# Performance work log

Measured on AMD Instinct MI355X. Metric: run time of the kernel, lower is better.

## Reference

```python
import jax, jax.numpy as jnp
import numpy as np

N = 100000
FEAT = 256
HID = 128
OUT = 64
E = 1600000


def setup_inputs() -> dict:
    key = jax.random.key(0)
    ks = jax.random.split(key, 8)
    x = jax.random.normal(ks[0], (N, FEAT), dtype=jnp.float32)
    edge_index = jax.random.randint(ks[1], (2, E), 0, N, dtype=jnp.int64)
    # Glorot-like weights, zero bias (PyG GCNConv default init style)
    def glorot(k, fin, fout):
        s = (6.0 / (fin + fout)) ** 0.5
        return jax.random.uniform(k, (fin, fout), jnp.float32, -s, s)
    return {
        "x": x,
        "edge_index": edge_index,
        "W1": glorot(ks[2], FEAT, HID), "b1": jnp.zeros((HID,), jnp.float32),
        "W2": glorot(ks[3], HID, HID), "b2": jnp.zeros((HID,), jnp.float32),
        "W3": glorot(ks[4], HID, OUT), "b3": jnp.zeros((OUT,), jnp.float32),
    }


def _gcn_prep(edge_index, n_nodes):
    # Add self-loops and compute symmetric normalization deg^-1/2 (PyG gcn_norm).
    loops = jnp.arange(n_nodes, dtype=edge_index.dtype)
    src = jnp.concatenate([edge_index[0], loops])
    dst = jnp.concatenate([edge_index[1], loops])
    ones = jnp.ones(src.shape[0], dtype=jnp.float32)
    deg = jax.ops.segment_sum(ones, dst, num_segments=n_nodes)
    dinv = jnp.where(deg > 0, jax.lax.rsqrt(jnp.maximum(deg, 1.0)), 0.0)
    norm = dinv[src] * dinv[dst]  # [E+N]
    return src, dst, norm


def _gcn_layer(x, src, dst, norm, W, b, n_nodes):
    h = x @ W                              # [N, F_out]
    msg = h[src] * norm[:, None]           # gather + edge scale
    out = jax.ops.segment_sum(msg, dst, num_segments=n_nodes)  # scatter-add
    return out + b


def reference(x, edge_index, W1, b1, W2, b2, W3, b3):
    n = x.shape[0]
    src, dst, norm = _gcn_prep(edge_index, n)
    h = jax.nn.relu(_gcn_layer(x, src, dst, norm, W1, b1, n))
    h = jax.nn.relu(_gcn_layer(h, src, dst, norm, W2, b2, n))
    return _gcn_layer(h, src, dst, norm, W3, b3, n)
```

## Files before the change

### kernel.cpp

```cpp
#include <hip/hip_runtime.h>
#include <hip/hip_bf16.h>


#define NNODES 100000
#define NB 391
#define PB 2048
#define BCAP 12288

typedef _Float16 half8  __attribute__((ext_vector_type(8)));
typedef _Float16 half4v __attribute__((ext_vector_type(4)));
typedef _Float16 half2v __attribute__((ext_vector_type(2)));
typedef float    floatx4 __attribute__((ext_vector_type(4)));

static __device__ __forceinline__ floatx4 h2f4(half4v v) {
    return (floatx4){(float)v.x, (float)v.y, (float)v.z, (float)v.w};
}

__global__ __launch_bounds__(256) void blockhist_k(const int* __restrict__ dst,
                                                   int* __restrict__ H, int e) {
    __shared__ int h[NB];
    for (int q = threadIdx.x; q < NB; q += 256) h[q] = 0;
    __syncthreads();
    int base = blockIdx.x * PB;
    int lim = e - base; if (lim > PB) lim = PB;
    for (int i = threadIdx.x; i < lim; i += 256)
        atomicAdd(&h[dst[base + i] >> 8], 1);
    __syncthreads();
    for (int q = threadIdx.x; q < NB; q += 256)
        H[(size_t)blockIdx.x * NB + q] = h[q];
}

__global__ __launch_bounds__(256) void bucketscan_k(const int* __restrict__ H,
                                                    int* __restrict__ O,
                                                    int* __restrict__ T, int npb) {
    __shared__ int lds[256];
    int b = blockIdx.x, t = threadIdx.x;
    int running = 0;
    for (int c0 = 0; c0 < npb; c0 += 256) {
        int idx = c0 + t;
        int v = (idx < npb) ? H[(size_t)idx * NB + b] : 0;
        lds[t] = v;
        __syncthreads();
        #pragma unroll
        for (int off = 1; off < 256; off <<= 1) {
            int u = (t >= off) ? lds[t - off] : 0;
            __syncthreads();
            lds[t] += u;
            __syncthreads();
        }
        int excl = lds[t] - v + running;
        if (idx < npb) O[(size_t)idx * NB + b] = excl;
        running += lds[255];
        __syncthreads();
    }
    if (t == 0) T[b] = running;
}

__global__ __launch_bounds__(512) void scanT_k(const int* __restrict__ T,
                                               int* __restrict__ bbase, int e) {
    __shared__ int lds[512];
    int t = threadIdx.x;
    int v = (t < NB) ? T[t] : 0;
    lds[t] = v;
    __syncthreads();
    #pragma unroll
    for (int off = 1; off < 512; off <<= 1) {
        int u = (t >= off) ? lds[t - off] : 0;
        __syncthreads();
        lds[t] += u;
        __syncthreads();
    }
    if (t < NB) bbase[t] = lds[t] - v;
    if (t == 0) bbase[NB] = e;
}

__global__ __launch_bounds__(256) void scatter_k(const int* __restrict__ src,
                                                 const int* __restrict__ dst,
                                                 const int* __restrict__ O,
                                                 const int* __restrict__ bbase,
                                                 unsigned* __restrict__ binned, int e) {
    __shared__ int cur[NB];
    for (int q = threadIdx.x; q < NB; q += 256)
        cur[q] = bbase[q] + O[(size_t)blockIdx.x * NB + q];
    __syncthreads();
    int base = blockIdx.x * PB;
    int lim = e - base; if (lim > PB) lim = PB;
    for (int i = threadIdx.x; i < lim; i += 256) {
        int d = dst[base + i];
        int s = src[base + i];
        int p = atomicAdd(&cur[d >> 8], 1);
        binned[p] = ((unsigned)(d & 255) << 17) | (unsigned)s;
    }
}

__global__ __launch_bounds__(256) void bucket_fill_k(
    const unsigned* __restrict__ binned, const int* __restrict__ bbase,
    int* __restrict__ rowptr, int* __restrict__ eidx,
    float* __restrict__ dinv, int n, int e) {
    __shared__ int cnt[256];
    __shared__ int cur[256];
    __shared__ int lds[256];
    __shared__ int sbuf[BCAP];
    int b = blockIdx.x, t = threadIdx.x;
    int beg = bbase[b], end = bbase[b + 1];
    int m = end - beg;
    cnt[t] = 0;
    __syncthreads();
    for (int q = t; q < m; q += 256) {
        unsigned r = binned[beg + q];
        atomicAdd(&cnt[r >> 17], 1);
    }
    __syncthreads();
    int v = cnt[t];
    lds[t] = v;
    __syncthreads();
    #pragma unroll
    for (int off = 1; off < 256; off <<= 1) {
        int u = (t >= off) ? lds[t - off] : 0;
        __syncthreads();
        lds[t] += u;
        __syncthreads();
    }
    int excl = lds[t] - v;
    int node = b * 256 + t;
    if (node < n) {
        rowptr[node] = beg + excl;
        dinv[node] = rsqrtf(1.0f + (float)v);
    }
    if (b == NB - 1 && t == 0) rowptr[n] = e;
    cur[t] = excl;
    __syncthreads();
    for (int q = t; q < m; q += 256) {
        unsigned r = binned[beg + q];
        int p = atomicAdd(&cur[r >> 17], 1);
        if (p < BCAP) sbuf[p] = (int)(r & 0x1FFFFu);
    }
    __syncthreads();
    for (int q = t; q < m; q += 256) eidx[beg + q] = sbuf[q];
}

template<typename TA, int FIN, int FOUT>
__global__ __launch_bounds__(256) void gemm_mfma_k(
    const TA* __restrict__ X, const float* __restrict__ W,
    const float* __restrict__ dinv, _Float16* __restrict__ G, int n)
{
    constexpr int KC = (FIN > 128) ? 128 : FIN;
    constexpr int KP = KC + 8;
    constexpr int NT = FOUT / 16;
    __shared__ _Float16 wT[FOUT * KP];

    const int tid  = threadIdx.x;
    const int wave = tid >> 6;
    const int lane = tid & 63;
    const int mrow = lane & 15;
    const int kq   = (lane >> 4) * 8;

    const int m0 = blockIdx.x * 128 + wave * 32;
    int r0 = m0 + mrow;      if (r0 > n - 1) r0 = n - 1;
    int r1 = m0 + 16 + mrow; if (r1 > n - 1) r1 = n - 1;

    floatx4 acc[2][NT];
    #pragma unroll
    for (int i = 0; i < 2; ++i)
        #pragma unroll
        for (int j = 0; j < NT; ++j) acc[i][j] = (floatx4){0.f, 0.f, 0.f, 0.f};

    for (int kc = 0; kc < FIN; kc += KC) {
        if (kc) __syncthreads();
        for (int q = tid; q < KC * FOUT; q += 256) {
            int k = q / FOUT, nn = q % FOUT;
            wT[nn * KP + k] = (_Float16)W[(size_t)(kc + k) * FOUT + nn];
        }
        __syncthreads();

        #pragma unroll
        for (int kk = 0; kk < KC; kk += 32) {
            half8 a0, a1;
            if constexpr (sizeof(TA) == 2) {
                const _Float16* xp = (const _Float16*)X;
                a0 = *(const half8*)(xp + (size_t)r0 * FIN + kc + kk + kq);
                a1 = *(const half8*)(xp + (size_t)r1 * FIN + kc + kk + kq);
            } else {
                const float* xp0 = (const float*)X + (size_t)r0 * FIN + kc + kk + kq;
                const float* xp1 = (const float*)X + (size_t)r1 * FIN + kc + kk + kq;
                float4 u0 = *(const float4*)xp0, u1 = *(const float4*)(xp0 + 4);
                float4 v0 = *(const float4*)xp1, v1 = *(const float4*)(xp1 + 4);
                a0 = (half8){(_Float16)u0.x, (_Float16)u0.y, (_Float16)u0.z, (_Float16)u0.w,
                             (_Float16)u1.x, (_Float16)u1.y, (_Float16)u1.z, (_Float16)u1.w};
                a1 = (half8){(_Float16)v0.x, (_Float16)v0.y, (_Float16)v0.z, (_Float16)v0.w,
                             (_Float16)v1.x, (_Float16)v1.y, (_Float16)v1.z, (_Float16)v1.w};
            }
            #pragma unroll
            for (int ct = 0; ct < NT; ++ct) {
                half8 b = *(const half8*)&wT[(ct * 16 + mrow) * KP + kk + kq];
                acc[0][ct] = __builtin_amdgcn_mfma_f32_16x16x32_f16(a0, b, acc[0][ct], 0, 0, 0);
                acc[1][ct] = __builtin_amdgcn_mfma_f32_16x16x32_f16(a1, b, acc[1][ct], 0, 0, 0);
            }
        }
    }

    #pragma unroll
    for (int rt = 0; rt < 2; ++rt) {
        #pragma unroll
        for (int reg = 0; reg < 4; ++reg) {
            int r = m0 + rt * 16 + (lane >> 4) * 4 + reg;
            if (r < n) {
                float s = dinv[r];
                #pragma unroll
                for (int ct = 0; ct < NT; ++ct) {
                    G[(size_t)r * FOUT + ct * 16 + mrow] = (_Float16)(acc[rt][ct][reg] * s);
                }
            }
        }
    }
}

template<bool RELU, typename OutT>
__global__ __launch_bounds__(256) void gather128_k(
    const _Float16* __restrict__ g, const int* __restrict__ rowptr,
    const int* __restrict__ eidx, const float* __restrict__ dinv,
    const float* __restrict__ bias, OutT* __restrict__ out, int n)
{
    int wave = threadIdx.x >> 6;
    int lane = threadIdx.x & 63;
    int half = lane >> 5;
    int hl   = lane & 31;
    int node = blockIdx.x * 4 + wave;
    if (node >= n) return;

    int beg = rowptr[node];
    int end = rowptr[node + 1];

    const half4v* g4 = (const half4v*)g;
    floatx4 aA = {0.f,0.f,0.f,0.f}, aB = aA, aC = aA, aD = aA;
    if (half == 0) aA = h2f4(g4[(size_t)node * 32 + hl]);

    for (int j0 = beg; j0 < end; j0 += 64) {
        int m = end - j0; if (m > 64) m = 64;
        int id = (lane < m) ? eidx[j0 + lane] : 0;
        int t = 0;
        for (; t + 7 < m; t += 8) {
            int i0 = __shfl(id, t + half);
            int i1 = __shfl(id, t + 2 + half);
            int i2 = __shfl(id, t + 4 + half);
            int i3 = __shfl(id, t + 6 + half);
            half4v v0 = g4[(size_t)i0 * 32 + hl];
            half4v v1 = g4[(size_t)i1 * 32 + hl];
            half4v v2 = g4[(size_t)i2 * 32 + hl];
            half4v v3 = g4[(size_t)i3 * 32 + hl];
            aA += h2f4(v0); aB += h2f4(v1); aC += h2f4(v2); aD += h2f4(v3);
        }
        for (; t + 1 < m; t += 2) {
            int i0 = __shfl(id, t + half);
            aA += h2f4(g4[(size_t)i0 * 32 + hl]);
        }
        if (t < m) {
            int i0 = __shfl(id, t);
            if (half == 0) aA += h2f4(g4[(size_t)i0 * 32 + hl]);
        }
    }
    aA += aB; aC += aD; aA += aC;
    aA.x += __shfl_down(aA.x, 32);
    aA.y += __shfl_down(aA.y, 32);
    aA.z += __shfl_down(aA.z, 32);
    aA.w += __shfl_down(aA.w, 32);

    if (half == 0) {
        float sc = dinv[node];
        float4 bb = *(const float4*)(bias + 4 * hl);
        float o0 = fmaf(aA.x, sc, bb.x);
        float o1 = fmaf(aA.y, sc, bb.y);
        float o2 = fmaf(aA.z, sc, bb.z);
        float o3 = fmaf(aA.w, sc, bb.w);
        if (RELU) {
            o0 = fmaxf(o0, 0.f); o1 = fmaxf(o1, 0.f);
            o2 = fmaxf(o2, 0.f); o3 = fmaxf(o3, 0.f);
        }
        if constexpr (sizeof(OutT) == 2) {
            ((half4v*)out)[(size_t)node * 32 + hl] =
                (half4v){(_Float16)o0, (_Float16)o1, (_Float16)o2, (_Float16)o3};
        } else {
            *(float4*)((float*)out + (size_t)node * 128 + 4 * hl) =
                make_float4(o0, o1, o2, o3);
        }
    }
}

template<bool RELU>
__global__ __launch_bounds__(256) void gather64_k(
    const _Float16* __restrict__ g, const int* __restrict__ rowptr,
    const int* __restrict__ eidx, const float* __restrict__ dinv,
    const float* __restrict__ bias, float* __restrict__ out, int n)
{
    int wave = threadIdx.x >> 6;
    int lane = threadIdx.x & 63;
    int half = lane >> 5;
    int hl   = lane & 31;
    int node = blockIdx.x * 4 + wave;
    if (node >= n) return;

    int beg = rowptr[node];
    int end = rowptr[node + 1];

    const half2v* g2 = (const half2v*)g;
    float ax=0.f, ay=0.f, bx=0.f, by=0.f, cx=0.f, cy=0.f, dx=0.f, dy=0.f;
    if (half == 0) {
        half2v v = g2[(size_t)node * 32 + hl];
        ax = (float)v.x; ay = (float)v.y;
    }

    for (int j0 = beg; j0 < end; j0 += 64) {
        int m = end - j0; if (m > 64) m = 64;
        int id = (lane < m) ? eidx[j0 + lane] : 0;
        int t = 0;
        for (; t + 7 < m; t += 8) {
            int i0 = __shfl(id, t + half);
            int i1 = __shfl(id, t + 2 + half);
            int i2 = __shfl(id, t + 4 + half);
            int i3 = __shfl(id, t + 6 + half);
            half2v v0 = g2[(size_t)i0 * 32 + hl];
            half2v v1 = g2[(size_t)i1 * 32 + hl];
            half2v v2 = g2[(size_t)i2 * 32 + hl];
            half2v v3 = g2[(size_t)i3 * 32 + hl];
            ax += (float)v0.x; ay += (float)v0.y;
            bx += (float)v1.x; by += (float)v1.y;
            cx += (float)v2.x; cy += (float)v2.y;
            dx += (float)v3.x; dy += (float)v3.y;
        }
        for (; t + 1 < m; t += 2) {
            int i0 = __shfl(id, t + half);
            half2v v0 = g2[(size_t)i0 * 32 + hl];
            ax += (float)v0.x; ay += (float)v0.y;
        }
        if (t < m) {
            int i0 = __shfl(id, t);
            if (half == 0) {
                half2v v0 = g2[(size_t)i0 * 32 + hl];
                ax += (float)v0.x; ay += (float)v0.y;
            }
        }
    }
    ax += bx + cx + dx; ay += by + cy + dy;
    ax += __shfl_down(ax, 32);
    ay += __shfl_down(ay, 32);

    if (half == 0) {
        float sc = dinv[node];
        float2 bb = *(const float2*)(bias + 2 * hl);
        float ox = fmaf(ax, sc, bb.x);
        float oy = fmaf(ay, sc, bb.y);
        if (RELU) { ox = fmaxf(ox, 0.f); oy = fmaxf(oy, 0.f); }
        *(float2*)(out + (size_t)node * 64 + 2 * hl) = make_float2(ox, oy);
    }
}

extern "C" void kernel_launch(void* const* d_in, const int* in_sizes, int n_in,
                              void* d_out, int out_size, void* d_ws, size_t ws_size,
                              hipStream_t stream) {
    const float* x  = (const float*)d_in[0];
    const int*   ei = (const int*)d_in[1];
    const float* W1 = (const float*)d_in[2];
    const float* b1 = (const float*)d_in[3];
    const float* W2 = (const float*)d_in[4];
    const float* b2 = (const float*)d_in[5];
    const float* W3 = (const float*)d_in[6];
    const float* b3 = (const float*)d_in[7];
    float* out = (float*)d_out;

    const int N = NNODES;
    const int E = in_sizes[1] / 2;
    const int* srcI = ei;
    const int* dstI = ei + E;

    const int npb = (E + PB - 1) / PB;

    char* ws = (char*)d_ws;
    size_t p = 0;
    auto alloc = [&](size_t bytes) { void* r = ws + p; p = (p + bytes + 255) & ~(size_t)255; return r; };
    float*     dinv   = (float*)    alloc((size_t)N * 4);
    int*       rowptr = (int*)      alloc((size_t)(N + 1) * 4);
    int*       bbase  = (int*)      alloc((size_t)(NB + 1) * 4);
    int*       T      = (int*)      alloc((size_t)NB * 4);
    int*       H      = (int*)      alloc((size_t)npb * NB * 4);
    int*       O      = (int*)      alloc((size_t)npb * NB * 4);
    unsigned*  binned = (unsigned*) alloc((size_t)E * 4);
    int*       eidx   = (int*)      alloc((size_t)E * 4);
    _Float16*  A      = (_Float16*) alloc((size_t)N * 128 * 2);
    _Float16*  Ch     = (_Float16*) alloc((size_t)N * 128 * 2);

    const int nb_node4 = (N + 3) / 4;
    const int nb_gemm = (N + 127) / 128;

    blockhist_k<<<npb, 256, 0, stream>>>(dstI, H, E);
    bucketscan_k<<<NB, 256, 0, stream>>>(H, O, T, npb);
    scanT_k<<<1, 512, 0, stream>>>(T, bbase, E);
    scatter_k<<<npb, 256, 0, stream>>>(srcI, dstI, O, bbase, binned, E);
    bucket_fill_k<<<NB, 256, 0, stream>>>(binned, bbase, rowptr, eidx, dinv, N, E);

    gemm_mfma_k<float, 256, 128><<<nb_gemm, 256, 0, stream>>>(x, W1, dinv, A, N);
    gather128_k<true, _Float16><<<nb_node4, 256, 0, stream>>>(A, rowptr, eidx, dinv, b1, Ch, N);

    gemm_mfma_k<_Float16, 128, 128><<<nb_gemm, 256, 0, stream>>>(Ch, W2, dinv, A, N);
    gather128_k<true, _Float16><<<nb_node4, 256, 0, stream>>>(A, rowptr, eidx, dinv, b2, Ch, N);

    gemm_mfma_k<_Float16, 128, 64><<<nb_gemm, 256, 0, stream>>>(Ch, W3, dinv, A, N);
    gather64_k<false><<<nb_node4, 256, 0, stream>>>(A, rowptr, eidx, dinv, b3, out, N);
}
```

Before: 448.8 us.

## Pre-cast transposed fp16 weights once and stage X tiles in LDS for GEMM

Adds a small kernel that converts all three weight matrices to transposed fp16 once, instead of every GEMM block converting and transposing W into shared memory. The GEMM now stages coalesced row tiles of X (64-wide K chunks) in LDS and reads B fragments directly from the global fp16 weight buffer, which should stay cache-resident. This removes the per-block redundant weight conversion and the strided per-lane X loads. It adds an extra launch and more K-loop syncs, and B fragments now come from global/L2 rather than LDS.

```diff
diff --git a/kernel.cpp b/kernel.cpp
--- a/kernel.cpp
+++ b/kernel.cpp
@@ -139,15 +139,34 @@
     for (int q = t; q < m; q += 256) eidx[beg + q] = sbuf[q];
 }
 
+__global__ __launch_bounds__(256) void castWt_k(
+    const float* __restrict__ W1, const float* __restrict__ W2,
+    const float* __restrict__ W3, _Float16* __restrict__ Wt1,
+    _Float16* __restrict__ Wt2, _Float16* __restrict__ Wt3) {
+    int i = blockIdx.x * 256 + threadIdx.x;
+    if (i < 128 * 256) {
+        int nn = i >> 8, k = i & 255;
+        Wt1[i] = (_Float16)W1[k * 128 + nn];
+    }
+    if (i < 128 * 128) {
+        int nn = i >> 7, k = i & 127;
+        Wt2[i] = (_Float16)W2[k * 128 + nn];
+    }
+    if (i < 64 * 128) {
+        int nn = i >> 7, k = i & 127;
+        Wt3[i] = (_Float16)W3[k * 64 + nn];
+    }
+}
+
 template<typename TA, int FIN, int FOUT>
 __global__ __launch_bounds__(256) void gemm_mfma_k(
-    const TA* __restrict__ X, const float* __restrict__ W,
+    const TA* __restrict__ X, const _Float16* __restrict__ Wt,
     const float* __restrict__ dinv, _Float16* __restrict__ G, int n)
 {
-    constexpr int KC = (FIN > 128) ? 128 : FIN;
-    constexpr int KP = KC + 8;
+    constexpr int KC = 64;
+    constexpr int KP = 72;
     constexpr int NT = FOUT / 16;
-    __shared__ _Float16 wT[FOUT * KP];
+    __shared__ _Float16 xS[128 * KP];
 
     const int tid  = threadIdx.x;
     const int wave = tid >> 6;
@@ -155,9 +174,10 @@
     const int mrow = lane & 15;
     const int kq   = (lane >> 4) * 8;
 
-    const int m0 = blockIdx.x * 128 + wave * 32;
-    int r0 = m0 + mrow;      if (r0 > n - 1) r0 = n - 1;
-    int r1 = m0 + 16 + mrow; if (r1 > n - 1) r1 = n - 1;
+    const int m0 = blockIdx.x * 128;
+    const int row_s = tid >> 1;
+    const int col_s = (tid & 1) * 32;
+    int gr = m0 + row_s; if (gr > n - 1) gr = n - 1;
 
     floatx4 acc[2][NT];
     #pragma unroll
@@ -165,34 +185,37 @@
         #pragma unroll
         for (int j = 0; j < NT; ++j) acc[i][j] = (floatx4){0.f, 0.f, 0.f, 0.f};
 
+    const int lr0 = wave * 32 + mrow;
+    const int lr1 = lr0 + 16;
+
     for (int kc = 0; kc < FIN; kc += KC) {
         if (kc) __syncthreads();
-        for (int q = tid; q < KC * FOUT; q += 256) {
-            int k = q / FOUT, nn = q % FOUT;
-            wT[nn * KP + k] = (_Float16)W[(size_t)(kc + k) * FOUT + nn];
+        _Float16* sp = &xS[row_s * KP + col_s];
+        if constexpr (sizeof(TA) == 4) {
+            const float* xp = (const float*)X + (size_t)gr * FIN + kc + col_s;
+            #pragma unroll
+            for (int q = 0; q < 4; ++q) {
+                float4 u0 = *(const float4*)(xp + q * 8);
+                float4 u1 = *(const float4*)(xp + q * 8 + 4);
+                *(half8*)(sp + q * 8) =
+                    (half8){(_Float16)u0.x, (_Float16)u0.y, (_Float16)u0.z, (_Float16)u0.w,
+                            (_Float16)u1.x, (_Float16)u1.y, (_Float16)u1.z, (_Float16)u1.w};
+            }
+        } else {
+            const _Float16* xp = (const _Float16*)X + (size_t)gr * FIN + kc + col_s;
+            #pragma unroll
+            for (int q = 0; q < 4; ++q)
+                *(half8*)(sp + q * 8) = *(const half8*)(xp + q * 8);
         }
         __syncthreads();
 
         #pragma unroll
         for (int kk = 0; kk < KC; kk += 32) {
-            half8 a0, a1;
-            if constexpr (sizeof(TA) == 2) {
-                const _Float16* xp = (const _Float16*)X;
-                a0 = *(const half8*)(xp + (size_t)r0 * FIN + kc + kk + kq);
-                a1 = *(const half8*)(xp + (size_t)r1 * FIN + kc + kk + kq);
-            } else {
-                const float* xp0 = (const float*)X + (size_t)r0 * FIN + kc + kk + kq;
-                const float* xp1 = (const float*)X + (size_t)r1 * FIN + kc + kk + kq;
-                float4 u0 = *(const float4*)xp0, u1 = *(const float4*)(xp0 + 4);
-                float4 v0 = *(const float4*)xp1, v1 = *(const float4*)(xp1 + 4);
-                a0 = (half8){(_Float16)u0.x, (_Float16)u0.y, (_Float16)u0.z, (_Float16)u0.w,
-                             (_Float16)u1.x, (_Float16)u1.y, (_Float16)u1.z, (_Float16)u1.w};
-                a1 = (half8){(_Float16)v0.x, (_Float16)v0.y, (_Float16)v0.z, (_Float16)v0.w,
-                             (_Float16)v1.x, (_Float16)v1.y, (_Float16)v1.z, (_Float16)v1.w};
-            }
+            half8 a0 = *(const half8*)&xS[lr0 * KP + kk + kq];
+            half8 a1 = *(const half8*)&xS[lr1 * KP + kk + kq];
             #pragma unroll
             for (int ct = 0; ct < NT; ++ct) {
-                half8 b = *(const half8*)&wT[(ct * 16 + mrow) * KP + kk + kq];
+                half8 b = *(const half8*)(Wt + (size_t)(ct * 16 + mrow) * FIN + kc + kk + kq);
                 acc[0][ct] = __builtin_amdgcn_mfma_f32_16x16x32_f16(a0, b, acc[0][ct], 0, 0, 0);
                 acc[1][ct] = __builtin_amdgcn_mfma_f32_16x16x32_f16(a1, b, acc[1][ct], 0, 0, 0);
             }
@@ -203,7 +226,7 @@
     for (int rt = 0; rt < 2; ++rt) {
         #pragma unroll
         for (int reg = 0; reg < 4; ++reg) {
-            int r = m0 + rt * 16 + (lane >> 4) * 4 + reg;
+            int r = m0 + wave * 32 + rt * 16 + (lane >> 4) * 4 + reg;
             if (r < n) {
                 float s = dinv[r];
                 #pragma unroll
@@ -385,6 +408,9 @@
     int*       O      = (int*)      alloc((size_t)npb * NB * 4);
     unsigned*  binned = (unsigned*) alloc((size_t)E * 4);
     int*       eidx   = (int*)      alloc((size_t)E * 4);
+    _Float16*  Wt1    = (_Float16*) alloc((size_t)128 * 256 * 2);
+    _Float16*  Wt2    = (_Float16*) alloc((size_t)128 * 128 * 2);
+    _Float16*  Wt3    = (_Float16*) alloc((size_t)64 * 128 * 2);
     _Float16*  A      = (_Float16*) alloc((size_t)N * 128 * 2);
     _Float16*  Ch     = (_Float16*) alloc((size_t)N * 128 * 2);
 
@@ -392,17 +418,18 @@
     const int nb_gemm = (N + 127) / 128;
 
     blockhist_k<<<npb, 256, 0, stream>>>(dstI, H, E);
+    castWt_k<<<128, 256, 0, stream>>>(W1, W2, W3, Wt1, Wt2, Wt3);
     bucketscan_k<<<NB, 256, 0, stream>>>(H, O, T, npb);
     scanT_k<<<1, 512, 0, stream>>>(T, bbase, E);
     scatter_k<<<npb, 256, 0, stream>>>(srcI, dstI, O, bbase, binned, E);
     bucket_fill_k<<<NB, 256, 0, stream>>>(binned, bbase, rowptr, eidx, dinv, N, E);
 
-    gemm_mfma_k<float, 256, 128><<<nb_gemm, 256, 0, stream>>>(x, W1, dinv, A, N);
+    gemm_mfma_k<float, 256, 128><<<nb_gemm, 256, 0, stream>>>(x, Wt1, dinv, A, N);
     gather128_k<true, _Float16><<<nb_node4, 256, 0, stream>>>(A, rowptr, eidx, dinv, b1, Ch, N);
 
-    gemm_mfma_k<_Float16, 128, 128><<<nb_gemm, 256, 0, stream>>>(Ch, W2, dinv, A, N);
+    gemm_mfma_k<_Float16, 128, 128><<<nb_gemm, 256, 0, stream>>>(Ch, Wt2, dinv, A, N);
     gather128_k<true, _Float16><<<nb_node4, 256, 0, stream>>>(A, rowptr, eidx, dinv, b2, Ch, N);
 
-    gemm_mfma_k<_Float16, 128, 64><<<nb_gemm, 256, 0, stream>>>(Ch, W3, dinv, A, N);
+    gemm_mfma_k<_Float16, 128, 64><<<nb_gemm, 256, 0, stream>>>(Ch, Wt3, dinv, A, N);
     gather64_k<false><<<nb_node4, 256, 0, stream>>>(A, rowptr, eidx, dinv, b3, out, N);
 }
```

Result: slower. 476.5 us (+6.2%).
